# Kernel optimization log

Hardware: AMD Instinct MI355X
Metric: run time of the kernel (lower is better)

## Reference

```python
import jax, jax.numpy as jnp
import numpy as np

N = 1024
IN_CH = 128
EDGE_CH = 32
OUT_CH = 128


def setup_inputs() -> dict:
    key = jax.random.key(0)
    ks = jax.random.split(key, 8)
    return {
        "node_mat": jax.random.normal(ks[0], (N, IN_CH), dtype=jnp.float32),
        "adj": jax.random.uniform(ks[1], (N, N), dtype=jnp.float32),
        "edge_adj": jax.random.uniform(ks[2], (EDGE_CH, N, N), dtype=jnp.float32),
        "node_weight": jax.random.normal(ks[3], (IN_CH, OUT_CH), dtype=jnp.float32) * 0.05,
        "edge_lay_1": jax.random.normal(ks[4], (EDGE_CH, OUT_CH - 1), dtype=jnp.float32) * 0.05,
        "edge_lay_2": jax.random.normal(ks[5], (OUT_CH - 1, OUT_CH), dtype=jnp.float32) * 0.05,
        "root": jax.random.normal(ks[6], (IN_CH, OUT_CH), dtype=jnp.float32) * 0.05,
        "bias": jax.random.normal(ks[7], (OUT_CH,), dtype=jnp.float32) * 0.05,
    }


def reference(node_mat, adj, edge_adj, node_weight, edge_lay_1, edge_lay_2, root, bias):
    # node message passing: adj-weighted sum of transformed node features  [N, out]
    sum_filter_node_msgs = adj @ (node_mat @ node_weight)
    # edge MLP: 2-layer with ReLU, applied over the edge-channel axis
    # edge_adj: [E, N, N]; edge_lay_1: [E, out-1] -> h1: [out-1, N, N]
    h1 = jnp.maximum(jnp.einsum('enm,eb->bnm', edge_adj, edge_lay_1), 0.0)
    # h1: [out-1, N, N]; edge_lay_2: [out-1, out] -> h2: [out, N, N]
    h2 = jnp.einsum('bnm,bo->onm', h1, edge_lay_2)
    # adjacency-weighted compression: e_compress[n, o] = sum_m h2[o, n, m] * adj[n, m]
    e_compress = jnp.einsum('onm,nm->no', h2, adj)
    root_info = node_mat @ root
    return sum_filter_node_msgs + e_compress + root_info + bias
```

## Files before the change

### kernel.cpp

```cpp
#include <hip/hip_runtime.h>
#include <hip/hip_bf16.h>

#define NN 1024
#define IN_CH 128
#define EDGE_CH 32
#define OUT_CH 128

typedef __attribute__((ext_vector_type(8))) short bf16x8;
typedef __attribute__((ext_vector_type(4))) float f32x4;

static __device__ __forceinline__ short f2bf(float f) {
    union { float f; unsigned u; } v; v.f = f;
    unsigned r = v.u + 0x7FFFu + ((v.u >> 16) & 1u);
    return (short)(r >> 16);
}

__global__ void node_gemm_kernel(const float* __restrict__ node_mat,
                                 const float* __restrict__ node_weight,
                                 const float* __restrict__ root,
                                 short* __restrict__ PT,
                                 float* __restrict__ R) {
    __shared__ float nm[2 * IN_CH];
    int tid = threadIdx.x;
    int n0 = blockIdx.x * 2;
    nm[tid] = node_mat[n0 * IN_CH + tid];
    __syncthreads();
    int o = tid & 127;
    int h = tid >> 7;
    const float* nr = &nm[h * IN_CH];
    float accp = 0.f, accr = 0.f;
#pragma unroll 8
    for (int c = 0; c < IN_CH; ++c) {
        float x = nr[c];
        accp += x * node_weight[c * OUT_CH + o];
        accr += x * root[c * OUT_CH + o];
    }
    R[(size_t)(n0 + h) * OUT_CH + o] = accr;
    PT[(size_t)o * NN + (n0 + h)] = f2bf(accp);
}

__global__ void edge_out_kernel(const float* __restrict__ edge_adj,
                                const float* __restrict__ adj,
                                const float* __restrict__ L1,
                                const float* __restrict__ L2,
                                const float* __restrict__ R,
                                const float* __restrict__ bias,
                                float* __restrict__ out) {
    int n = blockIdx.x;
    int tid = threadIdx.x;
    int wave = tid >> 6;
    int lane = tid & 63;
    int quad = lane >> 4;
    int col  = lane & 15;

    bf16x8 a_frag[8];
#pragma unroll
    for (int bt = 0; bt < 8; ++bt) {
        int b = bt * 16 + col;
#pragma unroll
        for (int j = 0; j < 8; ++j) {
            int e = quad * 8 + j;
            float v = (b < OUT_CH - 1) ? L1[e * (OUT_CH - 1) + b] : 0.0f;
            a_frag[bt][j] = f2bf(v);
        }
    }

    float g_acc[8][4];
#pragma unroll
    for (int bt = 0; bt < 8; ++bt)
#pragma unroll
        for (int r = 0; r < 4; ++r) g_acc[bt][r] = 0.0f;

    const float* adj_row = adj + (size_t)n * NN;
    const float* ea_base = edge_adj + (size_t)n * NN;

    for (int c = 0; c < 4; ++c) {
        int base = wave * 256 + c * 64;
        float adjv[4];
        bf16x8 bf[4];
#pragma unroll
        for (int s = 0; s < 4; ++s) {
            int m = base + s * 16 + col;
            adjv[s] = adj_row[m];
#pragma unroll
            for (int j = 0; j < 8; ++j) {
                size_t e = (size_t)(quad * 8 + j);
                bf[s][j] = f2bf(ea_base[e * (size_t)(NN * NN) + m]);
            }
        }
#pragma unroll
        for (int s = 0; s < 4; ++s) {
#pragma unroll
            for (int bt = 0; bt < 8; ++bt) {
                f32x4 d = __builtin_amdgcn_mfma_f32_16x16x32_bf16(
                    a_frag[bt], bf[s], (f32x4){0.f, 0.f, 0.f, 0.f}, 0, 0, 0);
#pragma unroll
                for (int r = 0; r < 4; ++r)
                    g_acc[bt][r] += fmaxf(d[r], 0.0f) * adjv[s];
            }
        }
    }

#pragma unroll
    for (int bt = 0; bt < 8; ++bt)
#pragma unroll
        for (int r = 0; r < 4; ++r) {
            float v = g_acc[bt][r];
            v += __shfl_xor(v, 1);
            v += __shfl_xor(v, 2);
            v += __shfl_xor(v, 4);
            v += __shfl_xor(v, 8);
            g_acc[bt][r] = v;
        }

    __shared__ float gred[4][OUT_CH];
    __shared__ float gs[OUT_CH];
    __shared__ float part[2][OUT_CH];
    if (col == 0) {
#pragma unroll
        for (int bt = 0; bt < 8; ++bt)
#pragma unroll
            for (int r = 0; r < 4; ++r)
                gred[wave][bt * 16 + quad * 4 + r] = g_acc[bt][r];
    }
    __syncthreads();
    if (tid < OUT_CH)
        gs[tid] = gred[0][tid] + gred[1][tid] + gred[2][tid] + gred[3][tid];
    __syncthreads();

    int o = tid & 127;
    int hf = tid >> 7;
    float acc = 0.f;
    int blo = hf * 64, bhi = hf ? 127 : 64;
#pragma unroll 8
    for (int b = blo; b < bhi; ++b)
        acc += gs[b] * L2[b * OUT_CH + o];
    part[hf][o] = acc;
    __syncthreads();
    if (tid < 128)
        out[(size_t)n * OUT_CH + tid] =
            part[0][tid] + part[1][tid] + R[(size_t)n * OUT_CH + tid] + bias[tid];
}

__global__ void adjp_kernel(const float* __restrict__ adj,
                            const short* __restrict__ PT,
                            float* __restrict__ out) {
    int blk = blockIdx.x;
    int nb = blk & 31;
    int kc = blk >> 5;
    int tid = threadIdx.x;
    int wave = tid >> 6;
    int lane = tid & 63;
    int quad = lane >> 4;
    int col  = lane & 15;
    int nh = wave & 1;
    int oh = wave >> 1;
    int n0 = nb * 32 + nh * 16;
    int k0 = kc * 64;

    f32x4 acc[4];
#pragma unroll
    for (int ot = 0; ot < 4; ++ot) acc[ot] = (f32x4){0.f, 0.f, 0.f, 0.f};

#pragma unroll
    for (int ks = 0; ks < 2; ++ks) {
        int k = k0 + ks * 32 + quad * 8;
        const float* ap = adj + (size_t)(n0 + col) * NN + k;
        bf16x8 a;
#pragma unroll
        for (int j = 0; j < 8; ++j) a[j] = f2bf(ap[j]);
#pragma unroll
        for (int ot = 0; ot < 4; ++ot) {
            int o = oh * 64 + ot * 16 + col;
            bf16x8 b = *(const bf16x8*)(PT + (size_t)o * NN + k);
            acc[ot] = __builtin_amdgcn_mfma_f32_16x16x32_bf16(a, b, acc[ot], 0, 0, 0);
        }
    }

#pragma unroll
    for (int ot = 0; ot < 4; ++ot)
#pragma unroll
        for (int r = 0; r < 4; ++r)
            atomicAdd(&out[(size_t)(n0 + quad * 4 + r) * OUT_CH + oh * 64 + ot * 16 + col],
                      acc[ot][r]);
}

extern "C" void kernel_launch(void* const* d_in, const int* in_sizes, int n_in,
                              void* d_out, int out_size, void* d_ws, size_t ws_size,
                              hipStream_t stream) {
    const float* node_mat    = (const float*)d_in[0];
    const float* adj         = (const float*)d_in[1];
    const float* edge_adj    = (const float*)d_in[2];
    const float* node_weight = (const float*)d_in[3];
    const float* edge_lay_1  = (const float*)d_in[4];
    const float* edge_lay_2  = (const float*)d_in[5];
    const float* root        = (const float*)d_in[6];
    const float* bias        = (const float*)d_in[7];
    float* out = (float*)d_out;

    short* PT = (short*)d_ws;
    float* R  = (float*)((char*)d_ws + OUT_CH * NN * sizeof(short));

    node_gemm_kernel<<<NN / 2, 256, 0, stream>>>(node_mat, node_weight, root, PT, R);
    edge_out_kernel<<<NN, 256, 0, stream>>>(edge_adj, adj, edge_lay_1, edge_lay_2,
                                            R, bias, out);
    adjp_kernel<<<512, 256, 0, stream>>>(adj, PT, out);
}
```

Before: 245.3 us.

## Software-pipeline edge_adj loads and reorder adj@P kernel to avoid atomics

The edge kernel now double-buffers its edge_adj and adj loads in registers, prefetching the next 32-column chunk while MFMAs run on the current one. This is meant to hide the global-memory latency of the dominant 128 MB edge_adj stream. The adj@P GEMM is reworked to do a full-K reduction per block through shared memory and to write out plus R plus bias directly, removing the float atomics. It now runs before the edge kernel, which adds its result with a plain read-modify-write of out. The larger register footprint from the prefetch buffers may reduce occupancy.

```diff
diff --git a/kernel.cpp b/kernel.cpp
--- a/kernel.cpp
+++ b/kernel.cpp
@@ -39,12 +39,54 @@
     PT[(size_t)o * NN + (n0 + h)] = f2bf(accp);
 }
 
+__global__ void adjp_kernel(const float* __restrict__ adj,
+                            const short* __restrict__ PT,
+                            const float* __restrict__ R,
+                            const float* __restrict__ bias,
+                            float* __restrict__ out) {
+    int nt = blockIdx.x >> 2;
+    int ob = (blockIdx.x & 3) * 32;
+    int tid = threadIdx.x;
+    int wave = tid >> 6;
+    int lane = tid & 63;
+    int quad = lane >> 4;
+    int col  = lane & 15;
+    int n0 = nt * 16;
+
+    f32x4 acc0 = {0.f, 0.f, 0.f, 0.f};
+    f32x4 acc1 = {0.f, 0.f, 0.f, 0.f};
+#pragma unroll 2
+    for (int ks = 0; ks < 8; ++ks) {
+        int k = wave * 256 + ks * 32 + quad * 8;
+        const float* ap = adj + (size_t)(n0 + col) * NN + k;
+        bf16x8 a;
+#pragma unroll
+        for (int j = 0; j < 8; ++j) a[j] = f2bf(ap[j]);
+        bf16x8 b0 = *(const bf16x8*)(PT + (size_t)(ob + col) * NN + k);
+        bf16x8 b1 = *(const bf16x8*)(PT + (size_t)(ob + 16 + col) * NN + k);
+        acc0 = __builtin_amdgcn_mfma_f32_16x16x32_bf16(a, b0, acc0, 0, 0, 0);
+        acc1 = __builtin_amdgcn_mfma_f32_16x16x32_bf16(a, b1, acc1, 0, 0, 0);
+    }
+
+    __shared__ float red[4][32][17];
+#pragma unroll
+    for (int r = 0; r < 4; ++r) {
+        red[wave][col][quad * 4 + r]      = acc0[r];
+        red[wave][16 + col][quad * 4 + r] = acc1[r];
+    }
+    __syncthreads();
+    for (int i = tid; i < 512; i += 256) {
+        int ol = i >> 4, nl = i & 15;
+        float v = red[0][ol][nl] + red[1][ol][nl] + red[2][ol][nl] + red[3][ol][nl];
+        int o = ob + ol, nr = n0 + nl;
+        out[(size_t)nr * OUT_CH + o] = v + R[(size_t)nr * OUT_CH + o] + bias[o];
+    }
+}
+
 __global__ void edge_out_kernel(const float* __restrict__ edge_adj,
                                 const float* __restrict__ adj,
                                 const float* __restrict__ L1,
                                 const float* __restrict__ L2,
-                                const float* __restrict__ R,
-                                const float* __restrict__ bias,
                                 float* __restrict__ out) {
     int n = blockIdx.x;
     int tid = threadIdx.x;
@@ -71,32 +113,49 @@
 #pragma unroll
         for (int r = 0; r < 4; ++r) g_acc[bt][r] = 0.0f;
 
-    const float* adj_row = adj + (size_t)n * NN;
-    const float* ea_base = edge_adj + (size_t)n * NN;
-
-    for (int c = 0; c < 4; ++c) {
-        int base = wave * 256 + c * 64;
-        float adjv[4];
-        bf16x8 bf[4];
-#pragma unroll
-        for (int s = 0; s < 4; ++s) {
-            int m = base + s * 16 + col;
-            adjv[s] = adj_row[m];
-#pragma unroll
-            for (int j = 0; j < 8; ++j) {
-                size_t e = (size_t)(quad * 8 + j);
-                bf[s][j] = f2bf(ea_base[e * (size_t)(NN * NN) + m]);
-            }
-        }
-#pragma unroll
-        for (int s = 0; s < 4; ++s) {
+    const float* base[8];
+#pragma unroll
+    for (int j = 0; j < 8; ++j)
+        base[j] = edge_adj + (size_t)(quad * 8 + j) * (size_t)(NN * NN)
+                + (size_t)n * NN + wave * 256 + col;
+    const float* abase = adj + (size_t)n * NN + wave * 256 + col;
+
+    float eb[2][16];
+    float av[2][2];
+
+#pragma unroll
+    for (int s = 0; s < 2; ++s) av[0][s] = abase[s * 16];
+#pragma unroll
+    for (int j = 0; j < 8; ++j)
+#pragma unroll
+        for (int s = 0; s < 2; ++s) eb[0][j * 2 + s] = base[j][s * 16];
+
+#pragma unroll
+    for (int c = 0; c < 8; ++c) {
+        int cur = c & 1, nxt = cur ^ 1;
+        if (c < 7) {
+            int off = (c + 1) * 32;
+#pragma unroll
+            for (int s = 0; s < 2; ++s) av[nxt][s] = abase[off + s * 16];
+#pragma unroll
+            for (int j = 0; j < 8; ++j)
+#pragma unroll
+                for (int s = 0; s < 2; ++s)
+                    eb[nxt][j * 2 + s] = base[j][off + s * 16];
+        }
+#pragma unroll
+        for (int s = 0; s < 2; ++s) {
+            bf16x8 bf;
+#pragma unroll
+            for (int j = 0; j < 8; ++j) bf[j] = f2bf(eb[cur][j * 2 + s]);
+            float a = av[cur][s];
 #pragma unroll
             for (int bt = 0; bt < 8; ++bt) {
                 f32x4 d = __builtin_amdgcn_mfma_f32_16x16x32_bf16(
-                    a_frag[bt], bf[s], (f32x4){0.f, 0.f, 0.f, 0.f}, 0, 0, 0);
+                    a_frag[bt], bf, (f32x4){0.f, 0.f, 0.f, 0.f}, 0, 0, 0);
 #pragma unroll
                 for (int r = 0; r < 4; ++r)
-                    g_acc[bt][r] += fmaxf(d[r], 0.0f) * adjv[s];
+                    g_acc[bt][r] += fmaxf(d[r], 0.0f) * a;
             }
         }
     }
@@ -138,51 +197,7 @@
     part[hf][o] = acc;
     __syncthreads();
     if (tid < 128)
-        out[(size_t)n * OUT_CH + tid] =
-            part[0][tid] + part[1][tid] + R[(size_t)n * OUT_CH + tid] + bias[tid];
-}
-
-__global__ void adjp_kernel(const float* __restrict__ adj,
-                            const short* __restrict__ PT,
-                            float* __restrict__ out) {
-    int blk = blockIdx.x;
-    int nb = blk & 31;
-    int kc = blk >> 5;
-    int tid = threadIdx.x;
-    int wave = tid >> 6;
-    int lane = tid & 63;
-    int quad = lane >> 4;
-    int col  = lane & 15;
-    int nh = wave & 1;
-    int oh = wave >> 1;
-    int n0 = nb * 32 + nh * 16;
-    int k0 = kc * 64;
-
-    f32x4 acc[4];
-#pragma unroll
-    for (int ot = 0; ot < 4; ++ot) acc[ot] = (f32x4){0.f, 0.f, 0.f, 0.f};
-
-#pragma unroll
-    for (int ks = 0; ks < 2; ++ks) {
-        int k = k0 + ks * 32 + quad * 8;
-        const float* ap = adj + (size_t)(n0 + col) * NN + k;
-        bf16x8 a;
-#pragma unroll
-        for (int j = 0; j < 8; ++j) a[j] = f2bf(ap[j]);
-#pragma unroll
-        for (int ot = 0; ot < 4; ++ot) {
-            int o = oh * 64 + ot * 16 + col;
-            bf16x8 b = *(const bf16x8*)(PT + (size_t)o * NN + k);
-            acc[ot] = __builtin_amdgcn_mfma_f32_16x16x32_bf16(a, b, acc[ot], 0, 0, 0);
-        }
-    }
-
-#pragma unroll
-    for (int ot = 0; ot < 4; ++ot)
-#pragma unroll
-        for (int r = 0; r < 4; ++r)
-            atomicAdd(&out[(size_t)(n0 + quad * 4 + r) * OUT_CH + oh * 64 + ot * 16 + col],
-                      acc[ot][r]);
+        out[(size_t)n * OUT_CH + tid] += part[0][tid] + part[1][tid];
 }
 
 extern "C" void kernel_launch(void* const* d_in, const int* in_sizes, int n_in,
@@ -202,7 +217,6 @@
     float* R  = (float*)((char*)d_ws + OUT_CH * NN * sizeof(short));
 
     node_gemm_kernel<<<NN / 2, 256, 0, stream>>>(node_mat, node_weight, root, PT, R);
-    edge_out_kernel<<<NN, 256, 0, stream>>>(edge_adj, adj, edge_lay_1, edge_lay_2,
-                                            R, bias, out);
-    adjp_kernel<<<512, 256, 0, stream>>>(adj, PT, out);
-}
+    adjp_kernel<<<256, 256, 0, stream>>>(adj, PT, R, bias, out);
+    edge_out_kernel<<<NN, 256, 0, stream>>>(edge_adj, adj, edge_lay_1, edge_lay_2, out);
+}
```

New measurement: 333.2 us. 1.36x slower.

## Double-buffer edge_adj via async LDS loads and fuse adj@P into edge kernel

Applied to the files above, without the earlier changes.

Stages edge_adj and the adj row into LDS with global_load_lds async copies, double-buffered so loads overlap the MFMA work. Waves now split the output channels instead of the m dimension, which removes the cross-wave reduction. The separate adj@P MFMA kernel with atomics is dropped and the product is computed as an fp32 dot over the cached adj row inside the fused kernel. node_gemm is rewritten with MFMA. The risks are extra per-block serial work reading PF (1024x128 floats per row block), and hand-written waitcnt encodings.

```diff
diff --git a/kernel.cpp b/kernel.cpp
--- a/kernel.cpp
+++ b/kernel.cpp
@@ -15,174 +15,173 @@
     return (short)(r >> 16);
 }
 
+static __device__ __forceinline__ void async_copy16(const float* gptr, float* lptr) {
+    __builtin_amdgcn_global_load_lds(
+        (const __attribute__((address_space(1))) void*)gptr,
+        (__attribute__((address_space(3))) void*)lptr,
+        16, 0, 0);
+}
+
 __global__ void node_gemm_kernel(const float* __restrict__ node_mat,
                                  const float* __restrict__ node_weight,
                                  const float* __restrict__ root,
-                                 short* __restrict__ PT,
+                                 float* __restrict__ PF,
                                  float* __restrict__ R) {
-    __shared__ float nm[2 * IN_CH];
     int tid = threadIdx.x;
-    int n0 = blockIdx.x * 2;
-    nm[tid] = node_mat[n0 * IN_CH + tid];
-    __syncthreads();
-    int o = tid & 127;
-    int h = tid >> 7;
-    const float* nr = &nm[h * IN_CH];
-    float accp = 0.f, accr = 0.f;
-#pragma unroll 8
-    for (int c = 0; c < IN_CH; ++c) {
-        float x = nr[c];
-        accp += x * node_weight[c * OUT_CH + o];
-        accr += x * root[c * OUT_CH + o];
-    }
-    R[(size_t)(n0 + h) * OUT_CH + o] = accr;
-    PT[(size_t)o * NN + (n0 + h)] = f2bf(accp);
-}
-
-__global__ void edge_out_kernel(const float* __restrict__ edge_adj,
-                                const float* __restrict__ adj,
-                                const float* __restrict__ L1,
-                                const float* __restrict__ L2,
-                                const float* __restrict__ R,
-                                const float* __restrict__ bias,
-                                float* __restrict__ out) {
+    int wave = tid >> 6, lane = tid & 63, quad = lane >> 4, col = lane & 15;
+    int m0 = blockIdx.x * 16;
+
+    f32x4 accP[2] = {{0.f,0.f,0.f,0.f},{0.f,0.f,0.f,0.f}};
+    f32x4 accR[2] = {{0.f,0.f,0.f,0.f},{0.f,0.f,0.f,0.f}};
+
+#pragma unroll
+    for (int ks = 0; ks < 4; ++ks) {
+        bf16x8 a;
+#pragma unroll
+        for (int j = 0; j < 8; ++j)
+            a[j] = f2bf(node_mat[(m0 + col) * IN_CH + ks * 32 + quad * 8 + j]);
+#pragma unroll
+        for (int t = 0; t < 2; ++t) {
+            int ob = (wave * 2 + t) * 16;
+            bf16x8 bw, br;
+#pragma unroll
+            for (int j = 0; j < 8; ++j) {
+                int k = ks * 32 + quad * 8 + j;
+                bw[j] = f2bf(node_weight[k * OUT_CH + ob + col]);
+                br[j] = f2bf(root[k * OUT_CH + ob + col]);
+            }
+            accP[t] = __builtin_amdgcn_mfma_f32_16x16x32_bf16(a, bw, accP[t], 0, 0, 0);
+            accR[t] = __builtin_amdgcn_mfma_f32_16x16x32_bf16(a, br, accR[t], 0, 0, 0);
+        }
+    }
+#pragma unroll
+    for (int t = 0; t < 2; ++t)
+#pragma unroll
+        for (int r = 0; r < 4; ++r) {
+            int m = m0 + quad * 4 + r;
+            int o = (wave * 2 + t) * 16 + col;
+            PF[(size_t)m * OUT_CH + o] = accP[t][r];
+            R[(size_t)m * OUT_CH + o]  = accR[t][r];
+        }
+}
+
+__global__ void __launch_bounds__(256)
+fused_kernel(const float* __restrict__ edge_adj,
+             const float* __restrict__ adj,
+             const float* __restrict__ L1,
+             const float* __restrict__ L2,
+             const float* __restrict__ PF,
+             const float* __restrict__ R,
+             const float* __restrict__ bias,
+             float* __restrict__ out) {
+    __shared__ float ea_lds[2][8 * 260];
+    __shared__ float adj_lds[NN];
+    __shared__ float gs[OUT_CH];
+    __shared__ float part[2][OUT_CH];
+
     int n = blockIdx.x;
     int tid = threadIdx.x;
-    int wave = tid >> 6;
-    int lane = tid & 63;
-    int quad = lane >> 4;
-    int col  = lane & 15;
-
-    bf16x8 a_frag[8];
-#pragma unroll
-    for (int bt = 0; bt < 8; ++bt) {
-        int b = bt * 16 + col;
+    int wave = tid >> 6, lane = tid & 63, quad = lane >> 4, col = lane & 15;
+
+    bf16x8 a_frag[2];
+#pragma unroll
+    for (int t = 0; t < 2; ++t) {
+        int b = wave * 32 + t * 16 + col;
 #pragma unroll
         for (int j = 0; j < 8; ++j) {
             int e = quad * 8 + j;
-            float v = (b < OUT_CH - 1) ? L1[e * (OUT_CH - 1) + b] : 0.0f;
-            a_frag[bt][j] = f2bf(v);
-        }
-    }
-
-    float g_acc[8][4];
-#pragma unroll
-    for (int bt = 0; bt < 8; ++bt)
-#pragma unroll
-        for (int r = 0; r < 4; ++r) g_acc[bt][r] = 0.0f;
-
-    const float* adj_row = adj + (size_t)n * NN;
-    const float* ea_base = edge_adj + (size_t)n * NN;
-
-    for (int c = 0; c < 4; ++c) {
-        int base = wave * 256 + c * 64;
-        float adjv[4];
-        bf16x8 bf[4];
+            a_frag[t][j] = (b < OUT_CH - 1) ? f2bf(L1[e * (OUT_CH - 1) + b]) : (short)0;
+        }
+    }
+    float g_acc[2][4] = {{0.f,0.f,0.f,0.f},{0.f,0.f,0.f,0.f}};
+
+    const float* gsrc = edge_adj + (size_t)n * NN;
+    size_t eoff0 = ((size_t)(2 * wave + 0) * 4 + (lane >> 4)) * (size_t)(NN * NN)
+                 + (size_t)((lane & 15) * 4);
+    size_t eoff1 = ((size_t)(2 * wave + 1) * 4 + (lane >> 4)) * (size_t)(NN * NN)
+                 + (size_t)((lane & 15) * 4);
+    float* dst0 = &ea_lds[0][(2 * wave + 0) * 260];
+    float* dst1 = &ea_lds[0][(2 * wave + 1) * 260];
+    float* dst0b = &ea_lds[1][(2 * wave + 0) * 260];
+    float* dst1b = &ea_lds[1][(2 * wave + 1) * 260];
+
+    async_copy16(gsrc + eoff0, dst0);
+    async_copy16(gsrc + eoff1, dst1);
+    async_copy16(adj + (size_t)n * NN + wave * 256 + lane * 4, &adj_lds[wave * 256]);
+    async_copy16(gsrc + eoff0 + 64, dst0b);
+    async_copy16(gsrc + eoff1 + 64, dst1b);
+
+    for (int c = 0; c < 16; ++c) {
+        if (c < 15) __builtin_amdgcn_s_waitcnt(0xF72);
+        else        __builtin_amdgcn_s_waitcnt(0xF70);
+        __syncthreads();
+
+        const float* eb = ea_lds[c & 1];
 #pragma unroll
         for (int s = 0; s < 4; ++s) {
-            int m = base + s * 16 + col;
-            adjv[s] = adj_row[m];
+            float adjv = adj_lds[c * 64 + s * 16 + col];
+            bf16x8 bf;
 #pragma unroll
             for (int j = 0; j < 8; ++j) {
-                size_t e = (size_t)(quad * 8 + j);
-                bf[s][j] = f2bf(ea_base[e * (size_t)(NN * NN) + m]);
+                int e = quad * 8 + j;
+                bf[j] = f2bf(eb[(e >> 2) * 260 + (e & 3) * 64 + s * 16 + col]);
             }
-        }
-#pragma unroll
-        for (int s = 0; s < 4; ++s) {
-#pragma unroll
-            for (int bt = 0; bt < 8; ++bt) {
+#pragma unroll
+            for (int t = 0; t < 2; ++t) {
                 f32x4 d = __builtin_amdgcn_mfma_f32_16x16x32_bf16(
-                    a_frag[bt], bf[s], (f32x4){0.f, 0.f, 0.f, 0.f}, 0, 0, 0);
+                    a_frag[t], bf, (f32x4){0.f, 0.f, 0.f, 0.f}, 0, 0, 0);
 #pragma unroll
                 for (int r = 0; r < 4; ++r)
-                    g_acc[bt][r] += fmaxf(d[r], 0.0f) * adjv[s];
+                    g_acc[t][r] += fmaxf(d[r], 0.0f) * adjv;
             }
         }
-    }
-
-#pragma unroll
-    for (int bt = 0; bt < 8; ++bt)
+        __syncthreads();
+
+        if (c < 14) {
+            int nc = c + 2;
+            float* d0 = &ea_lds[nc & 1][(2 * wave + 0) * 260];
+            float* d1 = &ea_lds[nc & 1][(2 * wave + 1) * 260];
+            async_copy16(gsrc + eoff0 + nc * 64, d0);
+            async_copy16(gsrc + eoff1 + nc * 64, d1);
+        }
+    }
+
+#pragma unroll
+    for (int t = 0; t < 2; ++t)
 #pragma unroll
         for (int r = 0; r < 4; ++r) {
-            float v = g_acc[bt][r];
+            float v = g_acc[t][r];
             v += __shfl_xor(v, 1);
             v += __shfl_xor(v, 2);
             v += __shfl_xor(v, 4);
             v += __shfl_xor(v, 8);
-            g_acc[bt][r] = v;
-        }
-
-    __shared__ float gred[4][OUT_CH];
-    __shared__ float gs[OUT_CH];
-    __shared__ float part[2][OUT_CH];
-    if (col == 0) {
-#pragma unroll
-        for (int bt = 0; bt < 8; ++bt)
-#pragma unroll
-            for (int r = 0; r < 4; ++r)
-                gred[wave][bt * 16 + quad * 4 + r] = g_acc[bt][r];
-    }
-    __syncthreads();
-    if (tid < OUT_CH)
-        gs[tid] = gred[0][tid] + gred[1][tid] + gred[2][tid] + gred[3][tid];
+            if (col == 0) gs[wave * 32 + t * 16 + quad * 4 + r] = v;
+        }
     __syncthreads();
 
     int o = tid & 127;
     int hf = tid >> 7;
     float acc = 0.f;
-    int blo = hf * 64, bhi = hf ? 127 : 64;
+    int blo = hf * 64, bhi = hf ? (OUT_CH - 1) : 64;
 #pragma unroll 8
     for (int b = blo; b < bhi; ++b)
         acc += gs[b] * L2[b * OUT_CH + o];
+
+    float a0 = 0.f, a1 = 0.f, a2 = 0.f, a3 = 0.f;
+    const float* pf = PF + (size_t)(hf * 512) * OUT_CH + o;
+    const float* aw = &adj_lds[hf * 512];
+    for (int mm = 0; mm < 512; mm += 4) {
+        a0 += aw[mm + 0] * pf[(size_t)(mm + 0) * OUT_CH];
+        a1 += aw[mm + 1] * pf[(size_t)(mm + 1) * OUT_CH];
+        a2 += aw[mm + 2] * pf[(size_t)(mm + 2) * OUT_CH];
+        a3 += aw[mm + 3] * pf[(size_t)(mm + 3) * OUT_CH];
+    }
+    acc += (a0 + a1) + (a2 + a3);
     part[hf][o] = acc;
     __syncthreads();
     if (tid < 128)
         out[(size_t)n * OUT_CH + tid] =
             part[0][tid] + part[1][tid] + R[(size_t)n * OUT_CH + tid] + bias[tid];
-}
-
-__global__ void adjp_kernel(const float* __restrict__ adj,
-                            const short* __restrict__ PT,
-                            float* __restrict__ out) {
-    int blk = blockIdx.x;
-    int nb = blk & 31;
-    int kc = blk >> 5;
-    int tid = threadIdx.x;
-    int wave = tid >> 6;
-    int lane = tid & 63;
-    int quad = lane >> 4;
-    int col  = lane & 15;
-    int nh = wave & 1;
-    int oh = wave >> 1;
-    int n0 = nb * 32 + nh * 16;
-    int k0 = kc * 64;
-
-    f32x4 acc[4];
-#pragma unroll
-    for (int ot = 0; ot < 4; ++ot) acc[ot] = (f32x4){0.f, 0.f, 0.f, 0.f};
-
-#pragma unroll
-    for (int ks = 0; ks < 2; ++ks) {
-        int k = k0 + ks * 32 + quad * 8;
-        const float* ap = adj + (size_t)(n0 + col) * NN + k;
-        bf16x8 a;
-#pragma unroll
-        for (int j = 0; j < 8; ++j) a[j] = f2bf(ap[j]);
-#pragma unroll
-        for (int ot = 0; ot < 4; ++ot) {
-            int o = oh * 64 + ot * 16 + col;
-            bf16x8 b = *(const bf16x8*)(PT + (size_t)o * NN + k);
-            acc[ot] = __builtin_amdgcn_mfma_f32_16x16x32_bf16(a, b, acc[ot], 0, 0, 0);
-        }
-    }
-
-#pragma unroll
-    for (int ot = 0; ot < 4; ++ot)
-#pragma unroll
-        for (int r = 0; r < 4; ++r)
-            atomicAdd(&out[(size_t)(n0 + quad * 4 + r) * OUT_CH + oh * 64 + ot * 16 + col],
-                      acc[ot][r]);
 }
 
 extern "C" void kernel_launch(void* const* d_in, const int* in_sizes, int n_in,
@@ -198,11 +197,10 @@
     const float* bias        = (const float*)d_in[7];
     float* out = (float*)d_out;
 
-    short* PT = (short*)d_ws;
-    float* R  = (float*)((char*)d_ws + OUT_CH * NN * sizeof(short));
-
-    node_gemm_kernel<<<NN / 2, 256, 0, stream>>>(node_mat, node_weight, root, PT, R);
-    edge_out_kernel<<<NN, 256, 0, stream>>>(edge_adj, adj, edge_lay_1, edge_lay_2,
-                                            R, bias, out);
-    adjp_kernel<<<512, 256, 0, stream>>>(adj, PT, out);
-}
+    float* PF = (float*)d_ws;
+    float* R  = PF + NN * OUT_CH;
+
+    node_gemm_kernel<<<64, 256, 0, stream>>>(node_mat, node_weight, root, PF, R);
+    fused_kernel<<<NN, 256, 0, stream>>>(edge_adj, adj, edge_lay_1, edge_lay_2,
+                                         PF, R, bias, out);
+}
```

Measured after the change: 262.4 us. +7.0%, slower.
